# Kernel optimization log

Hardware: AMD Instinct MI355X
Metric: run time of the kernel (lower is better)

Reference implementation:

```python
import jax, jax.numpy as jnp
import numpy as np

B = 262144
IN = 89          # obs(39) + one-hot task(50)
H = 64           # hidden_size
OUT = 8          # output_size
T = 50           # num_tasks


def setup_inputs() -> dict:
    key = jax.random.key(0)
    ks = jax.random.split(key, 10)
    s = 1.0 / np.sqrt(H)
    inputs = jax.random.normal(ks[0], (B, IN), dtype=jnp.float32)
    task_indices = jax.random.randint(ks[1], (B,), 0, T, dtype=jnp.int32)
    # trunk: 3 Linear+Tanh layers
    W0 = jax.random.normal(ks[2], (IN, H), dtype=jnp.float32) / np.sqrt(IN)
    b0 = jnp.zeros((H,), dtype=jnp.float32)
    W1 = jax.random.normal(ks[3], (H, H), dtype=jnp.float32) * s
    b1 = jnp.zeros((H,), dtype=jnp.float32)
    W2 = jax.random.normal(ks[4], (H, H), dtype=jnp.float32) * s
    b2 = jnp.zeros((H,), dtype=jnp.float32)
    # per-task output heads: num_task_layers=1 -> single Linear (no tanh)
    head_W = jax.random.normal(ks[5], (T, H, OUT), dtype=jnp.float32) * s
    head_b = jnp.zeros((T, OUT), dtype=jnp.float32)
    return {"inputs": inputs, "task_indices": task_indices,
            "W0": W0, "b0": b0, "W1": W1, "b1": b1, "W2": W2, "b2": b2,
            "head_W": head_W, "head_b": head_b}


def reference(inputs, task_indices, W0, b0, W1, b1, W2, b2, head_W, head_b):
    # Shared trunk: Linear + Tanh x3
    h = jnp.tanh(inputs @ W0 + b0)   # [B, H]
    h = jnp.tanh(h @ W1 + b1)
    h = jnp.tanh(h @ W2 + b2)
    # MoE-style dispatch/combine: gather per-sample head weights and apply.
    # Mathematically identical to partitioning by task, applying each head,
    # and scattering results back to original order.
    Wg = head_W[task_indices]        # [B, H, OUT]
    bg = head_b[task_indices]        # [B, OUT]
    out = jnp.einsum('bh,bho->bo', h, Wg) + bg  # [B, OUT]
    return out
```

## Files before the change

kernel.cpp:

```cpp
#include <hip/hip_runtime.h>
#include <stdint.h>
#include <stddef.h>


typedef _Float16 half8 __attribute__((ext_vector_type(8)));
typedef _Float16 half4 __attribute__((ext_vector_type(4)));
typedef _Float16 half2v __attribute__((ext_vector_type(2)));
typedef float    f32x4 __attribute__((ext_vector_type(4)));

constexpr int BN = 262144, INF = 89, HID = 64, OUTF = 8, NTASK = 50;
constexpr int NTHR = 128;
constexpr int ROWS = 64;
constexpr int XP   = 104;
constexpr int XTILE_F  = ROWS * INF;
constexpr int XTILE_V4 = XTILE_F / 4;

constexpr int W0F_OFF = 0;
constexpr int W1F_OFF = 12288;
constexpr int W2F_OFF = 20480;
constexpr int HWT_OFF = 28672;

__device__ __forceinline__ float fast_tanh(float v) {
    float e = __expf(2.0f * v);
    return 1.0f - 2.0f * __builtin_amdgcn_rcpf(e + 1.0f);
}

__device__ __forceinline__ float dot2acc(half2v a, half2v b, float c) {
#if __has_builtin(__builtin_amdgcn_fdot2)
    return __builtin_amdgcn_fdot2(a, b, c, false);
#else
    return fmaf((float)a[0], (float)b[0], fmaf((float)a[1], (float)b[1], c));
#endif
}

__global__ void prep_kernel(const float* __restrict__ W0, const float* __restrict__ W1,
                            const float* __restrict__ W2, const float* __restrict__ hW,
                            _Float16* __restrict__ ws) {
    const int tid = blockIdx.x * blockDim.x + threadIdx.x;
    const int stride = gridDim.x * blockDim.x;
    _Float16* w0f = ws + W0F_OFF / 2;
    _Float16* w1f = ws + W1F_OFF / 2;
    _Float16* w2f = ws + W2F_OFF / 2;
    _Float16* hwt = ws + HWT_OFF / 2;
    for (int i = tid; i < 3 * 4 * 64 * 8; i += stride) {
        int j = i & 7, l = (i >> 3) & 63, fk = i >> 9;
        int kk = fk >> 2, ft = fk & 3;
        int n = ft * 16 + (l & 15);
        int k = kk * 32 + (l >> 4) * 8 + j;
        w0f[i] = (_Float16)(k < INF ? W0[k * HID + n] : 0.0f);
    }
    for (int i = tid; i < 2 * 4 * 64 * 8; i += stride) {
        int j = i & 7, l = (i >> 3) & 63, fk = i >> 9;
        int kk = fk >> 2, ft = fk & 3;
        int n = ft * 16 + (l & 15);
        int k = kk * 32 + (l >> 4) * 8 + j;
        w1f[i] = (_Float16)W1[k * HID + n];
        w2f[i] = (_Float16)W2[k * HID + n];
    }
    for (int i = tid; i < NTASK * OUTF * HID; i += stride) {
        int t = i / (OUTF * HID), rem = i % (OUTF * HID);
        int o = rem / HID, k = rem % HID;
        hwt[i] = (_Float16)hW[(size_t)t * (HID * OUTF) + k * OUTF + o];
    }
}

__global__ __launch_bounds__(NTHR, 8) void mtn_mfma_kernel(
    const float* __restrict__ x,
    const int*   __restrict__ task,
    const float* __restrict__ b0, const float* __restrict__ b1,
    const float* __restrict__ b2,
    const float* __restrict__ hB,
    const _Float16* __restrict__ ws,
    float* __restrict__ out)
{
    __shared__ __align__(16) _Float16 xh[ROWS * XP];

    const int t = threadIdx.x;
    const int w = t >> 6;
    const int l = t & 63;
    const int c = l & 15;
    const int g = l >> 4;
    const int blockRow = blockIdx.x * ROWS;
    const int waveRow  = w * 32;

    const _Float16* w0f = ws + W0F_OFF / 2;
    const _Float16* w1f = ws + W1F_OFF / 2;
    const _Float16* w2f = ws + W2F_OFF / 2;
    const _Float16* hwt = ws + HWT_OFF / 2;

    const int jr = l >> 3, jo = l & 7;
    int   tks[4];
    float hBv[4];
    #pragma unroll
    for (int it = 0; it < 4; ++it)
        tks[it] = task[blockRow + waveRow + it * 8 + jr];
    #pragma unroll
    for (int it = 0; it < 4; ++it)
        hBv[it] = hB[tks[it] * OUTF + jo];

    {
        const float4* xb = reinterpret_cast<const float4*>(x + (size_t)blockRow * INF);
        #pragma unroll
        for (int i = 0; i < 12; ++i) {
            if (i < 11 || t < XTILE_V4 - 11 * NTHR) {
                float4 v = xb[t + i * NTHR];
                int e = 4 * (t + i * NTHR);
                #pragma unroll
                for (int q = 0; q < 4; ++q) {
                    int ee = e + q;
                    int rr = ee / INF, k = ee - rr * INF;
                    xh[rr * XP + k] = (_Float16)((q == 0) ? v.x : (q == 1) ? v.y
                                                 : (q == 2) ? v.z : v.w);
                }
            }
        }
        if (t < ROWS) {
            #pragma unroll
            for (int k = INF; k < 96; ++k) xh[t * XP + k] = (_Float16)0;
        }
    }
    __syncthreads();

    f32x4 acc[4][2];

    #pragma unroll
    for (int ft = 0; ft < 4; ++ft) {
        f32x4 bv = *(const f32x4*)(b0 + ft * 16 + g * 4);
        acc[ft][0] = bv; acc[ft][1] = bv;
    }
    #pragma unroll
    for (int kk = 0; kk < 3; ++kk) {
        half8 bf[2];
        #pragma unroll
        for (int bt = 0; bt < 2; ++bt)
            bf[bt] = *(const half8*)&xh[(waveRow + bt * 16 + c) * XP + kk * 32 + g * 8];
        #pragma unroll
        for (int ft = 0; ft < 4; ++ft) {
            half8 af = *(const half8*)(w0f + ((kk * 4 + ft) * 64 + l) * 8);
            acc[ft][0] = __builtin_amdgcn_mfma_f32_16x16x32_f16(af, bf[0], acc[ft][0], 0, 0, 0);
            acc[ft][1] = __builtin_amdgcn_mfma_f32_16x16x32_f16(af, bf[1], acc[ft][1], 0, 0, 0);
        }
    }
    #pragma unroll
    for (int ft = 0; ft < 4; ++ft)
        #pragma unroll
        for (int bt = 0; bt < 2; ++bt) {
            half4 hv;
            #pragma unroll
            for (int r = 0; r < 4; ++r) hv[r] = (_Float16)fast_tanh(acc[ft][bt][r]);
            *(half4*)&xh[(waveRow + bt * 16 + c) * XP + ft * 16 + g * 4] = hv;
        }

    #pragma unroll
    for (int layer = 0; layer < 2; ++layer) {
        const _Float16* WF  = layer ? w2f : w1f;
        const float*    bia = layer ? b2  : b1;
        #pragma unroll
        for (int ft = 0; ft < 4; ++ft) {
            f32x4 bv = *(const f32x4*)(bia + ft * 16 + g * 4);
            acc[ft][0] = bv; acc[ft][1] = bv;
        }
        #pragma unroll
        for (int kk = 0; kk < 2; ++kk) {
            half8 bf[2];
            #pragma unroll
            for (int bt = 0; bt < 2; ++bt)
                bf[bt] = *(const half8*)&xh[(waveRow + bt * 16 + c) * XP + kk * 32 + g * 8];
            #pragma unroll
            for (int ft = 0; ft < 4; ++ft) {
                half8 af = *(const half8*)(WF + ((kk * 4 + ft) * 64 + l) * 8);
                acc[ft][0] = __builtin_amdgcn_mfma_f32_16x16x32_f16(af, bf[0], acc[ft][0], 0, 0, 0);
                acc[ft][1] = __builtin_amdgcn_mfma_f32_16x16x32_f16(af, bf[1], acc[ft][1], 0, 0, 0);
            }
        }
        #pragma unroll
        for (int ft = 0; ft < 4; ++ft)
            #pragma unroll
            for (int bt = 0; bt < 2; ++bt) {
                half4 hv;
                #pragma unroll
                for (int r = 0; r < 4; ++r) hv[r] = (_Float16)fast_tanh(acc[ft][bt][r]);
                *(half4*)&xh[(waveRow + bt * 16 + c) * XP + ft * 16 + g * 4] = hv;
            }
    }

    #pragma unroll
    for (int it = 0; it < 4; ++it) {
        const int r = it * 8 + jr;
        const size_t grow = (size_t)blockRow + waveRow + r;
        const int tk = tks[it];
        const _Float16* wp = hwt + (size_t)tk * (OUTF * HID) + jo * 8;
        const half8 hv = *(const half8*)&xh[(waveRow + r) * XP + jo * 8];

        float p[8];
        #pragma unroll
        for (int o = 0; o < 8; ++o) {
            half8 wv = *(const half8*)(wp + o * HID);
            float a = 0.0f;
            #pragma unroll
            for (int pp = 0; pp < 4; ++pp) {
                half2v av = {hv[2 * pp], hv[2 * pp + 1]};
                half2v bv = {wv[2 * pp], wv[2 * pp + 1]};
                a = dot2acc(av, bv, a);
            }
            p[o] = a;
        }
        float t0 = p[0] + __shfl_xor(p[0], 1);
        float t1 = p[1] + __shfl_xor(p[1], 1);
        float t2 = p[2] + __shfl_xor(p[2], 1);
        float t3 = p[3] + __shfl_xor(p[3], 1);
        float t4 = p[4] + __shfl_xor(p[4], 1);
        float t5 = p[5] + __shfl_xor(p[5], 1);
        float t6 = p[6] + __shfl_xor(p[6], 1);
        float t7 = p[7] + __shfl_xor(p[7], 1);
        const bool b0s = (jo & 1) != 0;
        float s0 = b0s ? t1 : t0;
        float s1 = b0s ? t3 : t2;
        float s2 = b0s ? t5 : t4;
        float s3 = b0s ? t7 : t6;
        s0 += __shfl_xor(s0, 2);
        s1 += __shfl_xor(s1, 2);
        s2 += __shfl_xor(s2, 2);
        s3 += __shfl_xor(s3, 2);
        const bool b1s = (jo & 2) != 0;
        float u0 = b1s ? s1 : s0;
        float u1 = b1s ? s3 : s2;
        u0 += __shfl_xor(u0, 4);
        u1 += __shfl_xor(u1, 4);
        float res = ((jo & 4) ? u1 : u0) + hBv[it];
        out[grow * OUTF + jo] = res;
    }
}

extern "C" void kernel_launch(void* const* d_in, const int* in_sizes, int n_in,
                              void* d_out, int out_size, void* d_ws, size_t ws_size,
                              hipStream_t stream) {
    const float* x    = (const float*)d_in[0];
    const int*   task = (const int*)  d_in[1];
    const float* W0   = (const float*)d_in[2];
    const float* b0   = (const float*)d_in[3];
    const float* W1   = (const float*)d_in[4];
    const float* b1   = (const float*)d_in[5];
    const float* W2   = (const float*)d_in[6];
    const float* b2   = (const float*)d_in[7];
    const float* hW   = (const float*)d_in[8];
    const float* hB   = (const float*)d_in[9];
    float* out = (float*)d_out;
    _Float16* ws = (_Float16*)d_ws;

    prep_kernel<<<64, 256, 0, stream>>>(W0, W1, W2, hW, ws);
    mtn_mfma_kernel<<<BN / ROWS, NTHR, 0, stream>>>(x, task, b0, b1, b2, hB, ws, out);
}
```

Baseline: 43.88 us.

## Sort rows by task and split trunk and per-task head into separate kernels

Adds a counting sort of row indices by task (histogram, prefix, scatter kernels). The trunk output is written to a half-precision workspace buffer, and a separate head kernel then processes rows in task-sorted order so that neighbouring rows share head weights. This adds four extra launches plus a full round trip of the hidden activations through global memory. It also introduces atomic-based ordering and random gathers and scatters in the head kernel. When the workspace is too small it falls back to the original fused kernel.

```diff
diff --git a/kernel.cpp b/kernel.cpp
--- a/kernel.cpp
+++ b/kernel.cpp
@@ -12,13 +12,17 @@
 constexpr int NTHR = 128;
 constexpr int ROWS = 64;
 constexpr int XP   = 104;
-constexpr int XTILE_F  = ROWS * INF;
-constexpr int XTILE_V4 = XTILE_F / 4;
-
-constexpr int W0F_OFF = 0;
-constexpr int W1F_OFF = 12288;
-constexpr int W2F_OFF = 20480;
-constexpr int HWT_OFF = 28672;
+constexpr int XTILE_V4 = ROWS * INF / 4;
+
+constexpr int    W0F_OFF  = 0;
+constexpr int    W1F_OFF  = 12288;
+constexpr int    W2F_OFF  = 20480;
+constexpr int    HWT_OFF  = 28672;
+constexpr size_t H_OFF    = 79872;
+constexpr size_t IDX_OFF  = H_OFF + (size_t)BN * HID * 2;
+constexpr size_t HIST_OFF = IDX_OFF + (size_t)BN * 4;
+constexpr size_t BASE_OFF = HIST_OFF + 256;
+constexpr size_t WS_NEED  = BASE_OFF + 256;
 
 __device__ __forceinline__ float fast_tanh(float v) {
     float e = __expf(2.0f * v);
@@ -64,14 +68,60 @@
     }
 }
 
-__global__ __launch_bounds__(NTHR, 8) void mtn_mfma_kernel(
+__global__ void sort_init(int* __restrict__ hist, int* __restrict__ base) {
+    int t = threadIdx.x;
+    if (t < 64) { hist[t] = 0; base[t] = 0; }
+}
+
+__global__ __launch_bounds__(256) void sort_hist(const int* __restrict__ task,
+                                                 int* __restrict__ hist) {
+    __shared__ int lh[NTASK];
+    const int t = threadIdx.x;
+    if (t < NTASK) lh[t] = 0;
+    __syncthreads();
+    const int base = blockIdx.x * 1024;
+    #pragma unroll
+    for (int k = 0; k < 4; ++k) atomicAdd(&lh[task[base + t + k * 256]], 1);
+    __syncthreads();
+    if (t < NTASK) atomicAdd(&hist[t], lh[t]);
+}
+
+__global__ void sort_prefix(const int* __restrict__ hist, int* __restrict__ base) {
+    if (threadIdx.x == 0) {
+        int run = 0;
+        for (int i = 0; i < NTASK; ++i) { base[i] = run; run += hist[i]; }
+    }
+}
+
+__global__ __launch_bounds__(256) void sort_scatter(const int* __restrict__ task,
+                                                    int* __restrict__ base,
+                                                    int* __restrict__ idx) {
+    __shared__ int lcnt[NTASK];
+    __shared__ int lbase[NTASK];
+    const int t = threadIdx.x;
+    if (t < NTASK) lcnt[t] = 0;
+    __syncthreads();
+    const int rbase = blockIdx.x * 1024;
+    int tk[4], rank[4];
+    #pragma unroll
+    for (int k = 0; k < 4; ++k) {
+        tk[k] = task[rbase + t + k * 256];
+        rank[k] = atomicAdd(&lcnt[tk[k]], 1);
+    }
+    __syncthreads();
+    if (t < NTASK) lbase[t] = atomicAdd(&base[t], lcnt[t]);
+    __syncthreads();
+    #pragma unroll
+    for (int k = 0; k < 4; ++k)
+        idx[lbase[tk[k]] + rank[k]] = rbase + t + k * 256;
+}
+
+__global__ __launch_bounds__(NTHR, 8) void trunk_kernel(
     const float* __restrict__ x,
-    const int*   __restrict__ task,
     const float* __restrict__ b0, const float* __restrict__ b1,
     const float* __restrict__ b2,
-    const float* __restrict__ hB,
     const _Float16* __restrict__ ws,
-    float* __restrict__ out)
+    _Float16* __restrict__ hbuf)
 {
     __shared__ __align__(16) _Float16 xh[ROWS * XP];
 
@@ -86,17 +136,6 @@
     const _Float16* w0f = ws + W0F_OFF / 2;
     const _Float16* w1f = ws + W1F_OFF / 2;
     const _Float16* w2f = ws + W2F_OFF / 2;
-    const _Float16* hwt = ws + HWT_OFF / 2;
-
-    const int jr = l >> 3, jo = l & 7;
-    int   tks[4];
-    float hBv[4];
-    #pragma unroll
-    for (int it = 0; it < 4; ++it)
-        tks[it] = task[blockRow + waveRow + it * 8 + jr];
-    #pragma unroll
-    for (int it = 0; it < 4; ++it)
-        hBv[it] = hB[tks[it] * OUTF + jo];
 
     {
         const float4* xb = reinterpret_cast<const float4*>(x + (size_t)blockRow * INF);
@@ -184,13 +223,44 @@
             }
     }
 
+    const int jr = l >> 3, jo = l & 7;
     #pragma unroll
     for (int it = 0; it < 4; ++it) {
         const int r = it * 8 + jr;
         const size_t grow = (size_t)blockRow + waveRow + r;
+        half8 hv = *(const half8*)&xh[(waveRow + r) * XP + jo * 8];
+        *(half8*)(hbuf + grow * HID + jo * 8) = hv;
+    }
+}
+
+__global__ __launch_bounds__(256, 8) void head_kernel(
+    const int* __restrict__ idx,
+    const int* __restrict__ task,
+    const _Float16* __restrict__ ws,
+    const float* __restrict__ hB,
+    float* __restrict__ out)
+{
+    const int t = threadIdx.x;
+    const int w = t >> 6;
+    const int l = t & 63;
+    const int jr = l >> 3, jo = l & 7;
+    const int sbase = (blockIdx.x * 4 + w) * 32;
+    const _Float16* hwt  = ws + HWT_OFF / 2;
+    const _Float16* hbuf = ws + H_OFF / 2;
+
+    int rdx[4];
+    #pragma unroll
+    for (int it = 0; it < 4; ++it) rdx[it] = idx[sbase + it * 8 + jr];
+    int tks[4];
+    #pragma unroll
+    for (int it = 0; it < 4; ++it) tks[it] = task[rdx[it]];
+
+    #pragma unroll
+    for (int it = 0; it < 4; ++it) {
         const int tk = tks[it];
         const _Float16* wp = hwt + (size_t)tk * (OUTF * HID) + jo * 8;
-        const half8 hv = *(const half8*)&xh[(waveRow + r) * XP + jo * 8];
+        const half8 hv = *(const half8*)(hbuf + (size_t)rdx[it] * HID + jo * 8);
+        const float hb = hB[tk * OUTF + jo];
 
         float p[8];
         #pragma unroll
@@ -227,8 +297,160 @@
         float u1 = b1s ? s3 : s2;
         u0 += __shfl_xor(u0, 4);
         u1 += __shfl_xor(u1, 4);
-        float res = ((jo & 4) ? u1 : u0) + hBv[it];
-        out[grow * OUTF + jo] = res;
+        out[(size_t)rdx[it] * OUTF + jo] = ((jo & 4) ? u1 : u0) + hb;
+    }
+}
+
+__global__ __launch_bounds__(NTHR, 8) void fused_kernel(
+    const float* __restrict__ x, const int* __restrict__ task,
+    const float* __restrict__ b0, const float* __restrict__ b1,
+    const float* __restrict__ b2, const float* __restrict__ hB,
+    const _Float16* __restrict__ ws, float* __restrict__ out)
+{
+    __shared__ __align__(16) _Float16 xh[ROWS * XP];
+    const int t = threadIdx.x;
+    const int w = t >> 6;
+    const int l = t & 63;
+    const int c = l & 15;
+    const int g = l >> 4;
+    const int blockRow = blockIdx.x * ROWS;
+    const int waveRow  = w * 32;
+    const _Float16* w0f = ws + W0F_OFF / 2;
+    const _Float16* w1f = ws + W1F_OFF / 2;
+    const _Float16* w2f = ws + W2F_OFF / 2;
+    const _Float16* hwt = ws + HWT_OFF / 2;
+    const int jr = l >> 3, jo = l & 7;
+    int   tks[4];
+    float hBv[4];
+    #pragma unroll
+    for (int it = 0; it < 4; ++it) tks[it] = task[blockRow + waveRow + it * 8 + jr];
+    #pragma unroll
+    for (int it = 0; it < 4; ++it) hBv[it] = hB[tks[it] * OUTF + jo];
+    {
+        const float4* xb = reinterpret_cast<const float4*>(x + (size_t)blockRow * INF);
+        #pragma unroll
+        for (int i = 0; i < 12; ++i) {
+            if (i < 11 || t < XTILE_V4 - 11 * NTHR) {
+                float4 v = xb[t + i * NTHR];
+                int e = 4 * (t + i * NTHR);
+                #pragma unroll
+                for (int q = 0; q < 4; ++q) {
+                    int ee = e + q;
+                    int rr = ee / INF, k = ee - rr * INF;
+                    xh[rr * XP + k] = (_Float16)((q == 0) ? v.x : (q == 1) ? v.y
+                                                 : (q == 2) ? v.z : v.w);
+                }
+            }
+        }
+        if (t < ROWS) {
+            #pragma unroll
+            for (int k = INF; k < 96; ++k) xh[t * XP + k] = (_Float16)0;
+        }
+    }
+    __syncthreads();
+    f32x4 acc[4][2];
+    #pragma unroll
+    for (int ft = 0; ft < 4; ++ft) {
+        f32x4 bv = *(const f32x4*)(b0 + ft * 16 + g * 4);
+        acc[ft][0] = bv; acc[ft][1] = bv;
+    }
+    #pragma unroll
+    for (int kk = 0; kk < 3; ++kk) {
+        half8 bf[2];
+        #pragma unroll
+        for (int bt = 0; bt < 2; ++bt)
+            bf[bt] = *(const half8*)&xh[(waveRow + bt * 16 + c) * XP + kk * 32 + g * 8];
+        #pragma unroll
+        for (int ft = 0; ft < 4; ++ft) {
+            half8 af = *(const half8*)(w0f + ((kk * 4 + ft) * 64 + l) * 8);
+            acc[ft][0] = __builtin_amdgcn_mfma_f32_16x16x32_f16(af, bf[0], acc[ft][0], 0, 0, 0);
+            acc[ft][1] = __builtin_amdgcn_mfma_f32_16x16x32_f16(af, bf[1], acc[ft][1], 0, 0, 0);
+        }
+    }
+    #pragma unroll
+    for (int ft = 0; ft < 4; ++ft)
+        #pragma unroll
+        for (int bt = 0; bt < 2; ++bt) {
+            half4 hv;
+            #pragma unroll
+            for (int r = 0; r < 4; ++r) hv[r] = (_Float16)fast_tanh(acc[ft][bt][r]);
+            *(half4*)&xh[(waveRow + bt * 16 + c) * XP + ft * 16 + g * 4] = hv;
+        }
+    #pragma unroll
+    for (int layer = 0; layer < 2; ++layer) {
+        const _Float16* WF  = layer ? w2f : w1f;
+        const float*    bia = layer ? b2  : b1;
+        #pragma unroll
+        for (int ft = 0; ft < 4; ++ft) {
+            f32x4 bv = *(const f32x4*)(bia + ft * 16 + g * 4);
+            acc[ft][0] = bv; acc[ft][1] = bv;
+        }
+        #pragma unroll
+        for (int kk = 0; kk < 2; ++kk) {
+            half8 bf[2];
+            #pragma unroll
+            for (int bt = 0; bt < 2; ++bt)
+                bf[bt] = *(const half8*)&xh[(waveRow + bt * 16 + c) * XP + kk * 32 + g * 8];
+            #pragma unroll
+            for (int ft = 0; ft < 4; ++ft) {
+                half8 af = *(const half8*)(WF + ((kk * 4 + ft) * 64 + l) * 8);
+                acc[ft][0] = __builtin_amdgcn_mfma_f32_16x16x32_f16(af, bf[0], acc[ft][0], 0, 0, 0);
+                acc[ft][1] = __builtin_amdgcn_mfma_f32_16x16x32_f16(af, bf[1], acc[ft][1], 0, 0, 0);
+            }
+        }
+        #pragma unroll
+        for (int ft = 0; ft < 4; ++ft)
+            #pragma unroll
+            for (int bt = 0; bt < 2; ++bt) {
+                half4 hv;
+                #pragma unroll
+                for (int r = 0; r < 4; ++r) hv[r] = (_Float16)fast_tanh(acc[ft][bt][r]);
+                *(half4*)&xh[(waveRow + bt * 16 + c) * XP + ft * 16 + g * 4] = hv;
+            }
+    }
+    #pragma unroll
+    for (int it = 0; it < 4; ++it) {
+        const int r = it * 8 + jr;
+        const size_t grow = (size_t)blockRow + waveRow + r;
+        const int tk = tks[it];
+        const _Float16* wp = hwt + (size_t)tk * (OUTF * HID) + jo * 8;
+        const half8 hv = *(const half8*)&xh[(waveRow + r) * XP + jo * 8];
+        float p[8];
+        #pragma unroll
+        for (int o = 0; o < 8; ++o) {
+            half8 wv = *(const half8*)(wp + o * HID);
+            float a = 0.0f;
+            #pragma unroll
+            for (int pp = 0; pp < 4; ++pp) {
+                half2v av = {hv[2 * pp], hv[2 * pp + 1]};
+                half2v bv = {wv[2 * pp], wv[2 * pp + 1]};
+                a = dot2acc(av, bv, a);
+            }
+            p[o] = a;
+        }
+        float t0 = p[0] + __shfl_xor(p[0], 1);
+        float t1 = p[1] + __shfl_xor(p[1], 1);
+        float t2 = p[2] + __shfl_xor(p[2], 1);
+        float t3 = p[3] + __shfl_xor(p[3], 1);
+        float t4 = p[4] + __shfl_xor(p[4], 1);
+        float t5 = p[5] + __shfl_xor(p[5], 1);
+        float t6 = p[6] + __shfl_xor(p[6], 1);
+        float t7 = p[7] + __shfl_xor(p[7], 1);
+        const bool b0s = (jo & 1) != 0;
+        float s0 = b0s ? t1 : t0;
+        float s1 = b0s ? t3 : t2;
+        float s2 = b0s ? t5 : t4;
+        float s3 = b0s ? t7 : t6;
+        s0 += __shfl_xor(s0, 2);
+        s1 += __shfl_xor(s1, 2);
+        s2 += __shfl_xor(s2, 2);
+        s3 += __shfl_xor(s3, 2);
+        const bool b1s = (jo & 2) != 0;
+        float u0 = b1s ? s1 : s0;
+        float u1 = b1s ? s3 : s2;
+        u0 += __shfl_xor(u0, 4);
+        u1 += __shfl_xor(u1, 4);
+        out[grow * OUTF + jo] = ((jo & 4) ? u1 : u0) + hBv[it];
     }
 }
 
@@ -249,5 +471,22 @@
     _Float16* ws = (_Float16*)d_ws;
 
     prep_kernel<<<64, 256, 0, stream>>>(W0, W1, W2, hW, ws);
-    mtn_mfma_kernel<<<BN / ROWS, NTHR, 0, stream>>>(x, task, b0, b1, b2, hB, ws, out);
-}
+
+    if (ws_size < WS_NEED) {
+        fused_kernel<<<BN / ROWS, NTHR, 0, stream>>>(x, task, b0, b1, b2, hB, ws, out);
+        return;
+    }
+
+    char* wsb = (char*)d_ws;
+    int*  hist = (int*)(wsb + HIST_OFF);
+    int*  base = (int*)(wsb + BASE_OFF);
+    int*  idx  = (int*)(wsb + IDX_OFF);
+    _Float16* hbuf = (_Float16*)(wsb + H_OFF);
+
+    sort_init   <<<1,   128, 0, stream>>>(hist, base);
+    sort_hist   <<<256, 256, 0, stream>>>(task, hist);
+    sort_prefix <<<1,    64, 0, stream>>>(hist, base);
+    sort_scatter<<<256, 256, 0, stream>>>(task, base, idx);
+    trunk_kernel<<<BN / ROWS, NTHR, 0, stream>>>(x, b0, b1, b2, ws, hbuf);
+    head_kernel <<<BN / 128, 256, 0, stream>>>(idx, task, ws, hB, out);
+}
```

Result: slower. 75.95 us (+73.1%).
